# Kernel tuning notes

Measured on AMD Instinct MI355X. Metric: run time of the kernel, lower is better.

The kernel has to match this reference:

```python
import jax, jax.numpy as jnp
import numpy as np

NQ = 6   # n_qubits
NL = 6   # n_layers
B = 32768
TWO_PI = 6.2831853


def _ry(state, wire, theta):
    # state: [B, 2^NQ] complex64, wire 0 = most significant bit (torchquantum convention)
    b = state.shape[0]
    left, right = 2 ** wire, 2 ** (NQ - 1 - wire)
    s = state.reshape(b, left, 2, right)
    c = jnp.cos(theta * 0.5)[:, None, None].astype(state.dtype)
    sn = jnp.sin(theta * 0.5)[:, None, None].astype(state.dtype)
    s0, s1 = s[:, :, 0], s[:, :, 1]
    out = jnp.stack([c * s0 - sn * s1, sn * s0 + c * s1], axis=2)
    return out.reshape(b, -1)


def _rz(state, wire, theta):
    b = state.shape[0]
    left, right = 2 ** wire, 2 ** (NQ - 1 - wire)
    s = state.reshape(b, left, 2, right)
    p0 = jnp.exp(-0.5j * theta)[:, None, None].astype(state.dtype)
    p1 = jnp.exp(0.5j * theta)[:, None, None].astype(state.dtype)
    out = jnp.stack([s[:, :, 0] * p0, s[:, :, 1] * p1], axis=2)
    return out.reshape(b, -1)


def _cnot(state, ctrl, tgt):
    b = state.shape[0]
    s = state.reshape((b,) + (2,) * NQ)
    c_ax = ctrl + 1
    t_ax_in_slice = tgt + 1 if tgt < ctrl else tgt  # target axis after removing ctrl axis
    s0 = jnp.take(s, 0, axis=c_ax)
    s1 = jnp.flip(jnp.take(s, 1, axis=c_ax), axis=t_ax_in_slice)
    out = jnp.stack([s0, s1], axis=c_ax)
    return out.reshape(b, -1)


def _encode(x):
    # SphericalEncodingLayer: theta = acos(z), phi = atan2(y,x) mod 2pi; ry(theta), rz(phi) on each wire
    b = x.shape[0]
    theta = jnp.arccos(jnp.clip(x[:, 2], -1.0, 1.0))
    phi = jnp.mod(jnp.arctan2(x[:, 1], x[:, 0]) + TWO_PI, TWO_PI)
    state = jnp.zeros((b, 2 ** NQ), dtype=jnp.complex64).at[:, 0].set(1.0)
    for i in range(NQ):
        state = _ry(state, i, theta)
        state = _rz(state, i, phi)
    return state


def _qlayer(state, p):
    # BatchedQLayer: per wire rz(p[:,2i]), ry(p[:,2i+1]); then CNOT ring
    for i in range(NQ):
        state = _rz(state, i, p[:, 2 * i])
        state = _ry(state, i, p[:, 2 * i + 1])
    for i in range(NQ - 1):
        state = _cnot(state, i, i + 1)
    state = _cnot(state, NQ - 1, 0)
    return state


def _pauli_z_signs():
    k = np.arange(2 ** NQ)
    bits = (k[None, :] >> (NQ - 1 - np.arange(NQ))[:, None]) & 1  # [NQ, 2^NQ]
    return jnp.asarray(1 - 2 * bits, dtype=jnp.float32)


def setup_inputs() -> dict:
    key = jax.random.key(0)
    k1, k2 = jax.random.split(key)
    x = jax.random.normal(k1, (B, 3), dtype=jnp.float32)
    x = x / jnp.linalg.norm(x, axis=1, keepdims=True)  # points on unit sphere
    weights = jax.random.uniform(k2, (B, NL * 2 * NQ), dtype=jnp.float32,
                                 minval=0.0, maxval=TWO_PI)
    return {"x": x, "weights": weights}


def reference(x, weights):
    state = _encode(x)
    pos = 0
    for _ in range(NL):
        state = _qlayer(state, weights[:, pos:pos + 2 * NQ])
        pos += 2 * NQ
    probs = jnp.abs(state) ** 2                      # [B, 2^NQ]
    exp_vals = probs @ _pauli_z_signs().T            # [B, NQ] MeasureAll(PauliZ)
    return jax.nn.sigmoid(exp_vals)                  # no classical post-processing
```

## Files before the change

### kernel.cpp

```cpp
#include <hip/hip_runtime.h>

#define NQ 6
#define NL 6
#define TSTRIDE 148


typedef float v2f __attribute__((ext_vector_type(2)));

template<int CTRL>
__device__ __forceinline__ float dppf(float x) {
    return __builtin_bit_cast(float,
        __builtin_amdgcn_update_dpp(0, __builtin_bit_cast(int, x), CTRL, 0xF, 0xF, true));
}
__device__ __forceinline__ float sx1(float x) { return dppf<0xB1>(x); }
__device__ __forceinline__ float sx2(float x) { return dppf<0x4E>(x); }
__device__ __forceinline__ float sx4(float x) { return dppf<0x1B>(dppf<0x141>(x)); }

__device__ __forceinline__ v2f fma2(v2f a, v2f b, v2f c) {
    return __builtin_elementwise_fma(a, b, c);
}
__device__ __forceinline__ v2f swap2(v2f a) { return __builtin_shufflevector(a, a, 1, 0); }

__device__ __forceinline__ v2f shuf2_1(v2f a) { return v2f{sx1(a.x), sx1(a.y)}; }
__device__ __forceinline__ v2f shuf2_2(v2f a) { return v2f{sx2(a.x), sx2(a.y)}; }
__device__ __forceinline__ v2f shuf2_4(v2f a) { return v2f{sx4(a.x), sx4(a.y)}; }

template<int Q>
__device__ __forceinline__ void rz2(v2f (&re)[4], v2f (&im)[4], float c, float s, int lane) {
    const v2f C = {c, c};
    if constexpr (Q < 3) {
        const int lm = 4 >> Q;
        const float s2 = (lane & lm) ? s : -s;
        const v2f S = {s2, s2};
        #pragma unroll
        for (int p = 0; p < 4; ++p) {
            const v2f nr = fma2(re[p], C, -(im[p] * S));
            im[p] = fma2(re[p], S, im[p] * C);
            re[p] = nr;
        }
    } else if constexpr (Q == 5) {
        const v2f S = {-s, s};
        #pragma unroll
        for (int p = 0; p < 4; ++p) {
            const v2f nr = fma2(re[p], C, -(im[p] * S));
            im[p] = fma2(re[p], S, im[p] * C);
            re[p] = nr;
        }
    } else {
        const v2f Sn = {-s, -s}, Sp = {s, s};
        #pragma unroll
        for (int p = 0; p < 4; ++p) {
            const v2f S = (((Q == 3) ? (p & 2) : (p & 1)) != 0) ? Sp : Sn;
            const v2f nr = fma2(re[p], C, -(im[p] * S));
            im[p] = fma2(re[p], S, im[p] * C);
            re[p] = nr;
        }
    }
}

template<int Q>
__device__ __forceinline__ void ry2(v2f (&re)[4], v2f (&im)[4], float c, float s, int lane) {
    const v2f C = {c, c};
    if constexpr (Q < 3) {
        const int lm = 4 >> Q;
        const float sg = (lane & lm) ? s : -s;
        const v2f SG = {sg, sg};
        #pragma unroll
        for (int p = 0; p < 4; ++p) {
            v2f ore, oim;
            if constexpr (Q == 0)      { ore = shuf2_4(re[p]); oim = shuf2_4(im[p]); }
            else if constexpr (Q == 1) { ore = shuf2_2(re[p]); oim = shuf2_2(im[p]); }
            else                       { ore = shuf2_1(re[p]); oim = shuf2_1(im[p]); }
            re[p] = fma2(C, re[p], SG * ore);
            im[p] = fma2(C, im[p], SG * oim);
        }
    } else if constexpr (Q == 3) {
        const v2f S = {s, s};
        #pragma unroll
        for (int p = 0; p < 2; ++p) {
            const v2f a0r = re[p], a0i = im[p], a1r = re[p+2], a1i = im[p+2];
            re[p]   = fma2(C, a0r, -(S * a1r));
            im[p]   = fma2(C, a0i, -(S * a1i));
            re[p+2] = fma2(S, a0r, C * a1r);
            im[p+2] = fma2(S, a0i, C * a1i);
        }
    } else if constexpr (Q == 4) {
        const v2f S = {s, s};
        #pragma unroll
        for (int p = 0; p < 4; p += 2) {
            const v2f a0r = re[p], a0i = im[p], a1r = re[p+1], a1i = im[p+1];
            re[p]   = fma2(C, a0r, -(S * a1r));
            im[p]   = fma2(C, a0i, -(S * a1i));
            re[p+1] = fma2(S, a0r, C * a1r);
            im[p+1] = fma2(S, a0i, C * a1i);
        }
    } else {
        const v2f SM = {-s, s};
        #pragma unroll
        for (int p = 0; p < 4; ++p) {
            re[p] = fma2(C, re[p], SM * swap2(re[p]));
            im[p] = fma2(C, im[p], SM * swap2(im[p]));
        }
    }
}

__device__ __forceinline__ void cnot_block(v2f (&re)[4], v2f (&im)[4], int lane) {
    const bool c01 = (lane & 4) != 0;
    #pragma unroll
    for (int p = 0; p < 4; ++p) {
        const v2f dr = shuf2_2(re[p]), di = shuf2_2(im[p]);
        re[p] = c01 ? dr : re[p];
        im[p] = c01 ? di : im[p];
    }
    const bool c12 = (lane & 2) != 0;
    #pragma unroll
    for (int p = 0; p < 4; ++p) {
        const v2f dr = shuf2_1(re[p]), di = shuf2_1(im[p]);
        re[p] = c12 ? dr : re[p];
        im[p] = c12 ? di : im[p];
    }
    const bool c23 = (lane & 1) != 0;
    #pragma unroll
    for (int p = 0; p < 2; ++p) {
        const v2f ar = re[p], ai = im[p], br = re[p+2], bi = im[p+2];
        re[p]   = c23 ? br : ar;  im[p]   = c23 ? bi : ai;
        re[p+2] = c23 ? ar : br;  im[p+2] = c23 ? ai : bi;
    }
    { v2f t;
      t = re[2]; re[2] = re[3]; re[3] = t;
      t = im[2]; im[2] = im[3]; im[3] = t; }
    re[1] = swap2(re[1]); im[1] = swap2(im[1]);
    re[3] = swap2(re[3]); im[3] = swap2(im[3]);
    #pragma unroll
    for (int p = 0; p < 4; ++p) {
        re[p].y = sx4(re[p].y);
        im[p].y = sx4(im[p].y);
    }
}

__global__ __launch_bounds__(256) void qsim_kernel(
    const float* __restrict__ x,
    const float* __restrict__ w,
    float* __restrict__ out,
    int batch)
{
    __shared__ float tbl[32 * TSTRIDE];
    __shared__ float outbuf[4][48];

    const int tid   = threadIdx.x;
    const int wavei = tid >> 6;
    const int lane  = tid & 63;
    const int sw    = lane >> 3;
    const int g     = lane & 7;
    const int S     = tid >> 3;
    const int b     = blockIdx.x * 32 + S;
    if (b >= batch) return;

    float* T = &tbl[S * TSTRIDE];

    {
        const float* wp = w + (size_t)b * (2 * NQ * NL);
        #pragma unroll
        for (int j = 0; j < 9; ++j) {
            const int A = g * 9 + j;
            float s, c;
            __sincosf(wp[A] * 0.5f, &s, &c);
            const int word = (A >> 1) * 4 + (A & 1) * 2;
            T[word]     = c;
            T[word + 1] = s;
        }
    }

    const float x0 = x[b * 3 + 0];
    const float x1 = x[b * 3 + 1];
    const float x2 = x[b * 3 + 2];
    const float z  = fminf(1.f, fmaxf(-1.f, x2));
    const float ct = sqrtf(0.5f * (1.f + z));
    const float st = sqrtf(0.5f * (1.f - z));
    const float rr = sqrtf(x0 * x0 + x1 * x1) + 1e-30f;
    const float cphi = x0 / rr;
    const float cp = sqrtf(fmaxf(0.f, 0.5f * (1.f + cphi)));
    float sp       = sqrtf(fmaxf(0.f, 0.5f * (1.f - cphi)));
    sp = (x1 < 0.f) ? -sp : sp;

    const float Ar = ct * cp, Ai = -ct * sp;
    const float Br = st * cp, Bi =  st * sp;

    float pr[7], pi_[7], qr[7], qi[7];
    pr[0] = 1.f; pi_[0] = 0.f; qr[0] = 1.f; qi[0] = 0.f;
    pr[1] = Ar;  pi_[1] = Ai;  qr[1] = Br;  qi[1] = Bi;
    #pragma unroll
    for (int p = 2; p <= 6; ++p) {
        pr[p]  = fmaf(pr[p-1], Ar, -(pi_[p-1] * Ai));
        pi_[p] = fmaf(pr[p-1], Ai,  pi_[p-1] * Ar);
        qr[p]  = fmaf(qr[p-1], Br, -(qi[p-1] * Bi));
        qi[p]  = fmaf(qr[p-1], Bi,  qi[p-1] * Br);
    }
    float cr[7], ci[7];
    #pragma unroll
    for (int p = 0; p <= 6; ++p) {
        cr[p] = fmaf(pr[6-p], qr[p], -(pi_[6-p] * qi[p]));
        ci[p] = fmaf(pr[6-p], qi[p],  pi_[6-p] * qr[p]);
    }
    const int  pg = __popc(g);
    const bool pb0 = (pg & 1) != 0, pb1 = (pg & 2) != 0;
    float ur[4], ui[4];
    #pragma unroll
    for (int j = 0; j < 4; ++j) {
        const float lr  = pb0 ? cr[j+1] : cr[j];
        const float li  = pb0 ? ci[j+1] : ci[j];
        const float hr2 = pb0 ? cr[j+3] : cr[j+2];
        const float hi2 = pb0 ? ci[j+3] : ci[j+2];
        ur[j] = pb1 ? hr2 : lr;
        ui[j] = pb1 ? hi2 : li;
    }
    v2f re[4], im[4];
    re[0] = v2f{ur[0], ur[1]};  im[0] = v2f{ui[0], ui[1]};
    re[1] = v2f{ur[1], ur[2]};  im[1] = v2f{ui[1], ui[2]};
    re[2] = v2f{ur[1], ur[2]};  im[2] = v2f{ui[1], ui[2]};
    re[3] = v2f{ur[2], ur[3]};  im[3] = v2f{ui[2], ui[3]};

    for (int l = 0; l < NL - 1; ++l) {
        const float4 c0 = *(const float4*)&T[l*24 +  0];
        const float4 c1 = *(const float4*)&T[l*24 +  4];
        const float4 c2 = *(const float4*)&T[l*24 +  8];
        const float4 c3 = *(const float4*)&T[l*24 + 12];
        const float4 c4 = *(const float4*)&T[l*24 + 16];
        const float4 c5 = *(const float4*)&T[l*24 + 20];
        rz2<0>(re, im, c0.x, c0.y, lane);  ry2<0>(re, im, c0.z, c0.w, lane);
        rz2<1>(re, im, c1.x, c1.y, lane);  ry2<1>(re, im, c1.z, c1.w, lane);
        rz2<2>(re, im, c2.x, c2.y, lane);  ry2<2>(re, im, c2.z, c2.w, lane);
        rz2<3>(re, im, c3.x, c3.y, lane);  ry2<3>(re, im, c3.z, c3.w, lane);
        rz2<4>(re, im, c4.x, c4.y, lane);  ry2<4>(re, im, c4.z, c4.w, lane);
        rz2<5>(re, im, c5.x, c5.y, lane);  ry2<5>(re, im, c5.z, c5.w, lane);
        cnot_block(re, im, lane);
    }
    {
        const int l = NL - 1;
        const float4 c0 = *(const float4*)&T[l*24 +  0];
        const float4 c1 = *(const float4*)&T[l*24 +  4];
        const float4 c2 = *(const float4*)&T[l*24 +  8];
        const float4 c3 = *(const float4*)&T[l*24 + 12];
        const float4 c4 = *(const float4*)&T[l*24 + 16];
        const float4 c5 = *(const float4*)&T[l*24 + 20];
        rz2<0>(re, im, c0.x, c0.y, lane);  ry2<0>(re, im, c0.z, c0.w, lane);
        rz2<1>(re, im, c1.x, c1.y, lane);  ry2<1>(re, im, c1.z, c1.w, lane);
        rz2<2>(re, im, c2.x, c2.y, lane);  ry2<2>(re, im, c2.z, c2.w, lane);
        rz2<3>(re, im, c3.x, c3.y, lane);  ry2<3>(re, im, c3.z, c3.w, lane);
        rz2<4>(re, im, c4.x, c4.y, lane);  ry2<4>(re, im, c4.z, c4.w, lane);
        rz2<5>(re, im, c5.x, c5.y, lane);  ry2<5>(re, im, c5.z, c5.w, lane);
    }

    v2f v[4];
    #pragma unroll
    for (int p = 0; p < 4; ++p) v[p] = fma2(re[p], re[p], im[p] * im[p]);
    {
        v2f a, bb;
        a = v[0]; bb = v[2]; v[0] = a + bb; v[2] = a - bb;
        a = v[1]; bb = v[3]; v[1] = a + bb; v[3] = a - bb;
    }
    {
        v2f a, bb;
        a = v[0]; bb = v[1]; v[0] = a + bb; v[1] = a - bb;
        a = v[2]; bb = v[3]; v[2] = a + bb; v[3] = a - bb;
    }
    {
        const v2f PM = {1.f, -1.f};
        #pragma unroll
        for (int p = 0; p < 4; ++p) v[p] = fma2(PM, v[p], swap2(v[p]));
    }
    {
        const float sg = (lane & 1) ? -1.f : 1.f;
        const v2f SG = {sg, sg};
        #pragma unroll
        for (int p = 0; p < 4; ++p) v[p] = fma2(SG, v[p], shuf2_1(v[p]));
    }
    {
        const float sg = (lane & 2) ? -1.f : 1.f;
        const v2f SG = {sg, sg};
        #pragma unroll
        for (int p = 0; p < 4; ++p) v[p] = fma2(SG, v[p], shuf2_2(v[p]));
    }
    {
        const float sg = (lane & 4) ? -1.f : 1.f;
        const v2f SG = {sg, sg};
        #pragma unroll
        for (int p = 0; p < 4; ++p) v[p] = fma2(SG, v[p], shuf2_4(v[p]));
    }

    if (g == 3) outbuf[wavei][sw * 6 + 0] = v[3].y;
    if (g == 6) outbuf[wavei][sw * 6 + 1] = v[0].x;
    if (g == 7) {
        outbuf[wavei][sw * 6 + 2] = v[0].x;
        outbuf[wavei][sw * 6 + 3] = v[2].x;
        outbuf[wavei][sw * 6 + 4] = v[3].x;
        outbuf[wavei][sw * 6 + 5] = v[3].y;
    }
    if (lane < 48) {
        const float ev = outbuf[wavei][lane];
        const long long oidx = (long long)(blockIdx.x * 32 + wavei * 8) * 6 + lane;
        if (oidx < (long long)batch * 6)
            out[oidx] = 1.f / (1.f + __expf(-ev));
    }
}

extern "C" void kernel_launch(void* const* d_in, const int* in_sizes, int n_in,
                              void* d_out, int out_size, void* d_ws, size_t ws_size,
                              hipStream_t stream) {
    const float* x = (const float*)d_in[0];
    const float* w = (const float*)d_in[1];
    float* out = (float*)d_out;
    const int batch = in_sizes[0] / 3;

    const int threads = 256;
    const int blocks = (batch + 31) / 32;
    qsim_kernel<<<blocks, threads, 0, stream>>>(x, w, out, batch);
}
```

Before: 26.23 us.

## Spread each sample's statevector over 16 lanes instead of 8

Each batch sample now uses 16 lanes holding 4 amplitudes each, down from 8 lanes holding 8. Gates on the top four qubits become cross-lane DPP shuffles, including a new row-half mirror shuffle, and the CNOT ring and measurement butterflies are rewritten to match. The launch bound now requests higher occupancy and blocks cover 16 samples, so there are twice as many blocks. This aims to cut per-thread register pressure and the serial dependency chain and to expose more parallelism, at the cost of more DPP traffic and duplicated per-sample encoding and sincos work across lanes.

```diff
diff --git a/kernel.cpp b/kernel.cpp
--- a/kernel.cpp
+++ b/kernel.cpp
@@ -15,145 +15,134 @@
 __device__ __forceinline__ float sx1(float x) { return dppf<0xB1>(x); }
 __device__ __forceinline__ float sx2(float x) { return dppf<0x4E>(x); }
 __device__ __forceinline__ float sx4(float x) { return dppf<0x1B>(dppf<0x141>(x)); }
+__device__ __forceinline__ float sx8(float x) { return dppf<0x128>(x); }
 
 __device__ __forceinline__ v2f fma2(v2f a, v2f b, v2f c) {
     return __builtin_elementwise_fma(a, b, c);
 }
 __device__ __forceinline__ v2f swap2(v2f a) { return __builtin_shufflevector(a, a, 1, 0); }
 
-__device__ __forceinline__ v2f shuf2_1(v2f a) { return v2f{sx1(a.x), sx1(a.y)}; }
-__device__ __forceinline__ v2f shuf2_2(v2f a) { return v2f{sx2(a.x), sx2(a.y)}; }
-__device__ __forceinline__ v2f shuf2_4(v2f a) { return v2f{sx4(a.x), sx4(a.y)}; }
+template<int M>
+__device__ __forceinline__ v2f shuf2(v2f a) {
+    if constexpr (M == 1) return v2f{sx1(a.x), sx1(a.y)};
+    else if constexpr (M == 2) return v2f{sx2(a.x), sx2(a.y)};
+    else if constexpr (M == 4) return v2f{sx4(a.x), sx4(a.y)};
+    else return v2f{sx8(a.x), sx8(a.y)};
+}
 
 template<int Q>
-__device__ __forceinline__ void rz2(v2f (&re)[4], v2f (&im)[4], float c, float s, int lane) {
+__device__ __forceinline__ void rz2(v2f (&re)[2], v2f (&im)[2], float c, float s, int L) {
     const v2f C = {c, c};
-    if constexpr (Q < 3) {
-        const int lm = 4 >> Q;
-        const float s2 = (lane & lm) ? s : -s;
+    if constexpr (Q < 4) {
+        const int lm = 8 >> Q;
+        const float s2 = (L & lm) ? s : -s;
         const v2f S = {s2, s2};
         #pragma unroll
-        for (int p = 0; p < 4; ++p) {
+        for (int p = 0; p < 2; ++p) {
             const v2f nr = fma2(re[p], C, -(im[p] * S));
             im[p] = fma2(re[p], S, im[p] * C);
             re[p] = nr;
         }
-    } else if constexpr (Q == 5) {
+    } else if constexpr (Q == 4) {
+        const v2f Sn = {-s, -s}, Sp = {s, s};
+        { const v2f nr = fma2(re[0], C, -(im[0] * Sn));
+          im[0] = fma2(re[0], Sn, im[0] * C); re[0] = nr; }
+        { const v2f nr = fma2(re[1], C, -(im[1] * Sp));
+          im[1] = fma2(re[1], Sp, im[1] * C); re[1] = nr; }
+    } else {
         const v2f S = {-s, s};
         #pragma unroll
-        for (int p = 0; p < 4; ++p) {
+        for (int p = 0; p < 2; ++p) {
             const v2f nr = fma2(re[p], C, -(im[p] * S));
             im[p] = fma2(re[p], S, im[p] * C);
             re[p] = nr;
         }
-    } else {
-        const v2f Sn = {-s, -s}, Sp = {s, s};
-        #pragma unroll
-        for (int p = 0; p < 4; ++p) {
-            const v2f S = (((Q == 3) ? (p & 2) : (p & 1)) != 0) ? Sp : Sn;
-            const v2f nr = fma2(re[p], C, -(im[p] * S));
-            im[p] = fma2(re[p], S, im[p] * C);
-            re[p] = nr;
-        }
     }
 }
 
 template<int Q>
-__device__ __forceinline__ void ry2(v2f (&re)[4], v2f (&im)[4], float c, float s, int lane) {
+__device__ __forceinline__ void ry2(v2f (&re)[2], v2f (&im)[2], float c, float s, int L) {
     const v2f C = {c, c};
-    if constexpr (Q < 3) {
-        const int lm = 4 >> Q;
-        const float sg = (lane & lm) ? s : -s;
+    if constexpr (Q < 4) {
+        const int lm = 8 >> Q;
+        const float sg = (L & lm) ? s : -s;
         const v2f SG = {sg, sg};
         #pragma unroll
-        for (int p = 0; p < 4; ++p) {
-            v2f ore, oim;
-            if constexpr (Q == 0)      { ore = shuf2_4(re[p]); oim = shuf2_4(im[p]); }
-            else if constexpr (Q == 1) { ore = shuf2_2(re[p]); oim = shuf2_2(im[p]); }
-            else                       { ore = shuf2_1(re[p]); oim = shuf2_1(im[p]); }
+        for (int p = 0; p < 2; ++p) {
+            const v2f ore = shuf2<(8 >> Q)>(re[p]);
+            const v2f oim = shuf2<(8 >> Q)>(im[p]);
             re[p] = fma2(C, re[p], SG * ore);
             im[p] = fma2(C, im[p], SG * oim);
         }
-    } else if constexpr (Q == 3) {
-        const v2f S = {s, s};
-        #pragma unroll
-        for (int p = 0; p < 2; ++p) {
-            const v2f a0r = re[p], a0i = im[p], a1r = re[p+2], a1i = im[p+2];
-            re[p]   = fma2(C, a0r, -(S * a1r));
-            im[p]   = fma2(C, a0i, -(S * a1i));
-            re[p+2] = fma2(S, a0r, C * a1r);
-            im[p+2] = fma2(S, a0i, C * a1i);
-        }
     } else if constexpr (Q == 4) {
         const v2f S = {s, s};
-        #pragma unroll
-        for (int p = 0; p < 4; p += 2) {
-            const v2f a0r = re[p], a0i = im[p], a1r = re[p+1], a1i = im[p+1];
-            re[p]   = fma2(C, a0r, -(S * a1r));
-            im[p]   = fma2(C, a0i, -(S * a1i));
-            re[p+1] = fma2(S, a0r, C * a1r);
-            im[p+1] = fma2(S, a0i, C * a1i);
-        }
+        const v2f a0r = re[0], a0i = im[0], a1r = re[1], a1i = im[1];
+        re[0] = fma2(C, a0r, -(S * a1r));
+        im[0] = fma2(C, a0i, -(S * a1i));
+        re[1] = fma2(S, a0r, C * a1r);
+        im[1] = fma2(S, a0i, C * a1i);
     } else {
         const v2f SM = {-s, s};
         #pragma unroll
-        for (int p = 0; p < 4; ++p) {
+        for (int p = 0; p < 2; ++p) {
             re[p] = fma2(C, re[p], SM * swap2(re[p]));
             im[p] = fma2(C, im[p], SM * swap2(im[p]));
         }
     }
 }
 
-__device__ __forceinline__ void cnot_block(v2f (&re)[4], v2f (&im)[4], int lane) {
-    const bool c01 = (lane & 4) != 0;
-    #pragma unroll
-    for (int p = 0; p < 4; ++p) {
-        const v2f dr = shuf2_2(re[p]), di = shuf2_2(im[p]);
+__device__ __forceinline__ void cnot_block(v2f (&re)[2], v2f (&im)[2], int L) {
+    const bool c01 = (L & 8) != 0;
+    #pragma unroll
+    for (int p = 0; p < 2; ++p) {
+        const v2f dr = shuf2<4>(re[p]), di = shuf2<4>(im[p]);
         re[p] = c01 ? dr : re[p];
         im[p] = c01 ? di : im[p];
     }
-    const bool c12 = (lane & 2) != 0;
-    #pragma unroll
-    for (int p = 0; p < 4; ++p) {
-        const v2f dr = shuf2_1(re[p]), di = shuf2_1(im[p]);
+    const bool c12 = (L & 4) != 0;
+    #pragma unroll
+    for (int p = 0; p < 2; ++p) {
+        const v2f dr = shuf2<2>(re[p]), di = shuf2<2>(im[p]);
         re[p] = c12 ? dr : re[p];
         im[p] = c12 ? di : im[p];
     }
-    const bool c23 = (lane & 1) != 0;
-    #pragma unroll
-    for (int p = 0; p < 2; ++p) {
-        const v2f ar = re[p], ai = im[p], br = re[p+2], bi = im[p+2];
-        re[p]   = c23 ? br : ar;  im[p]   = c23 ? bi : ai;
-        re[p+2] = c23 ? ar : br;  im[p+2] = c23 ? ai : bi;
-    }
-    { v2f t;
-      t = re[2]; re[2] = re[3]; re[3] = t;
-      t = im[2]; im[2] = im[3]; im[3] = t; }
-    re[1] = swap2(re[1]); im[1] = swap2(im[1]);
-    re[3] = swap2(re[3]); im[3] = swap2(im[3]);
-    #pragma unroll
-    for (int p = 0; p < 4; ++p) {
-        re[p].y = sx4(re[p].y);
-        im[p].y = sx4(im[p].y);
-    }
-}
-
-__global__ __launch_bounds__(256) void qsim_kernel(
+    const bool c23 = (L & 2) != 0;
+    #pragma unroll
+    for (int p = 0; p < 2; ++p) {
+        const v2f dr = shuf2<1>(re[p]), di = shuf2<1>(im[p]);
+        re[p] = c23 ? dr : re[p];
+        im[p] = c23 ? di : im[p];
+    }
+    const bool c34 = (L & 1) != 0;
+    {
+        const v2f ar = re[0], ai = im[0], br = re[1], bi = im[1];
+        re[0] = c34 ? br : ar;  im[0] = c34 ? bi : ai;
+        re[1] = c34 ? ar : br;  im[1] = c34 ? ai : bi;
+    }
+    re[1] = swap2(re[1]);  im[1] = swap2(im[1]);
+    #pragma unroll
+    for (int p = 0; p < 2; ++p) {
+        re[p].y = sx8(re[p].y);
+        im[p].y = sx8(im[p].y);
+    }
+}
+
+__global__ __launch_bounds__(256, 8) void qsim_kernel(
     const float* __restrict__ x,
     const float* __restrict__ w,
     float* __restrict__ out,
     int batch)
 {
-    __shared__ float tbl[32 * TSTRIDE];
-    __shared__ float outbuf[4][48];
+    __shared__ float tbl[16 * TSTRIDE];
+    __shared__ float outbuf[4][24];
 
     const int tid   = threadIdx.x;
     const int wavei = tid >> 6;
     const int lane  = tid & 63;
-    const int sw    = lane >> 3;
-    const int g     = lane & 7;
-    const int S     = tid >> 3;
-    const int b     = blockIdx.x * 32 + S;
+    const int L     = lane & 15;
+    const int sw    = lane >> 4;
+    const int S     = tid >> 4;
+    const int b     = blockIdx.x * 16 + S;
     if (b >= batch) return;
 
     float* T = &tbl[S * TSTRIDE];
@@ -161,13 +150,15 @@
     {
         const float* wp = w + (size_t)b * (2 * NQ * NL);
         #pragma unroll
-        for (int j = 0; j < 9; ++j) {
-            const int A = g * 9 + j;
-            float s, c;
-            __sincosf(wp[A] * 0.5f, &s, &c);
-            const int word = (A >> 1) * 4 + (A & 1) * 2;
-            T[word]     = c;
-            T[word + 1] = s;
+        for (int j = 0; j < 5; ++j) {
+            const int A = L + 16 * j;
+            if (A < 72) {
+                float s, c;
+                __sincosf(wp[A] * 0.5f, &s, &c);
+                const int word = (A >> 1) * 4 + (A & 1) * 2;
+                T[word]     = c;
+                T[word + 1] = s;
+            }
         }
     }
 
@@ -202,106 +193,94 @@
         cr[p] = fmaf(pr[6-p], qr[p], -(pi_[6-p] * qi[p]));
         ci[p] = fmaf(pr[6-p], qi[p],  pi_[6-p] * qr[p]);
     }
-    const int  pg = __popc(g);
-    const bool pb0 = (pg & 1) != 0, pb1 = (pg & 2) != 0;
-    float ur[4], ui[4];
-    #pragma unroll
-    for (int j = 0; j < 4; ++j) {
-        const float lr  = pb0 ? cr[j+1] : cr[j];
-        const float li  = pb0 ? ci[j+1] : ci[j];
-        const float hr2 = pb0 ? cr[j+3] : cr[j+2];
-        const float hi2 = pb0 ? ci[j+3] : ci[j+2];
-        ur[j] = pb1 ? hr2 : lr;
-        ui[j] = pb1 ? hi2 : li;
-    }
-    v2f re[4], im[4];
+    const int  pg  = __popc(L);
+    const bool pb0 = (pg & 1) != 0, pb1 = (pg & 2) != 0, pb2 = (pg & 4) != 0;
+    float ur[3], ui[3];
+    #pragma unroll
+    for (int j = 0; j < 3; ++j) {
+        const float a01 = pb0 ? cr[j+1] : cr[j];
+        const float b01 = pb0 ? ci[j+1] : ci[j];
+        const float a23 = pb0 ? cr[j+3] : cr[j+2];
+        const float b23 = pb0 ? ci[j+3] : ci[j+2];
+        const float lor = pb1 ? a23 : a01;
+        const float loi = pb1 ? b23 : b01;
+        ur[j] = pb2 ? cr[j+4] : lor;
+        ui[j] = pb2 ? ci[j+4] : loi;
+    }
+    v2f re[2], im[2];
     re[0] = v2f{ur[0], ur[1]};  im[0] = v2f{ui[0], ui[1]};
     re[1] = v2f{ur[1], ur[2]};  im[1] = v2f{ui[1], ui[2]};
-    re[2] = v2f{ur[1], ur[2]};  im[2] = v2f{ui[1], ui[2]};
-    re[3] = v2f{ur[2], ur[3]};  im[3] = v2f{ui[2], ui[3]};
+
+    #define LAYER_GATES(l)                                                   \
+    do {                                                                     \
+        const float4 c0 = *(const float4*)&T[(l)*24 +  0];                   \
+        const float4 c1 = *(const float4*)&T[(l)*24 +  4];                   \
+        const float4 c2 = *(const float4*)&T[(l)*24 +  8];                   \
+        const float4 c3 = *(const float4*)&T[(l)*24 + 12];                   \
+        const float4 c4 = *(const float4*)&T[(l)*24 + 16];                   \
+        const float4 c5 = *(const float4*)&T[(l)*24 + 20];                   \
+        rz2<0>(re, im, c0.x, c0.y, L);  ry2<0>(re, im, c0.z, c0.w, L);       \
+        rz2<1>(re, im, c1.x, c1.y, L);  ry2<1>(re, im, c1.z, c1.w, L);       \
+        rz2<2>(re, im, c2.x, c2.y, L);  ry2<2>(re, im, c2.z, c2.w, L);       \
+        rz2<3>(re, im, c3.x, c3.y, L);  ry2<3>(re, im, c3.z, c3.w, L);       \
+        rz2<4>(re, im, c4.x, c4.y, L);  ry2<4>(re, im, c4.z, c4.w, L);       \
+        rz2<5>(re, im, c5.x, c5.y, L);  ry2<5>(re, im, c5.z, c5.w, L);       \
+    } while (0)
 
     for (int l = 0; l < NL - 1; ++l) {
-        const float4 c0 = *(const float4*)&T[l*24 +  0];
-        const float4 c1 = *(const float4*)&T[l*24 +  4];
-        const float4 c2 = *(const float4*)&T[l*24 +  8];
-        const float4 c3 = *(const float4*)&T[l*24 + 12];
-        const float4 c4 = *(const float4*)&T[l*24 + 16];
-        const float4 c5 = *(const float4*)&T[l*24 + 20];
-        rz2<0>(re, im, c0.x, c0.y, lane);  ry2<0>(re, im, c0.z, c0.w, lane);
-        rz2<1>(re, im, c1.x, c1.y, lane);  ry2<1>(re, im, c1.z, c1.w, lane);
-        rz2<2>(re, im, c2.x, c2.y, lane);  ry2<2>(re, im, c2.z, c2.w, lane);
-        rz2<3>(re, im, c3.x, c3.y, lane);  ry2<3>(re, im, c3.z, c3.w, lane);
-        rz2<4>(re, im, c4.x, c4.y, lane);  ry2<4>(re, im, c4.z, c4.w, lane);
-        rz2<5>(re, im, c5.x, c5.y, lane);  ry2<5>(re, im, c5.z, c5.w, lane);
-        cnot_block(re, im, lane);
-    }
-    {
-        const int l = NL - 1;
-        const float4 c0 = *(const float4*)&T[l*24 +  0];
-        const float4 c1 = *(const float4*)&T[l*24 +  4];
-        const float4 c2 = *(const float4*)&T[l*24 +  8];
-        const float4 c3 = *(const float4*)&T[l*24 + 12];
-        const float4 c4 = *(const float4*)&T[l*24 + 16];
-        const float4 c5 = *(const float4*)&T[l*24 + 20];
-        rz2<0>(re, im, c0.x, c0.y, lane);  ry2<0>(re, im, c0.z, c0.w, lane);
-        rz2<1>(re, im, c1.x, c1.y, lane);  ry2<1>(re, im, c1.z, c1.w, lane);
-        rz2<2>(re, im, c2.x, c2.y, lane);  ry2<2>(re, im, c2.z, c2.w, lane);
-        rz2<3>(re, im, c3.x, c3.y, lane);  ry2<3>(re, im, c3.z, c3.w, lane);
-        rz2<4>(re, im, c4.x, c4.y, lane);  ry2<4>(re, im, c4.z, c4.w, lane);
-        rz2<5>(re, im, c5.x, c5.y, lane);  ry2<5>(re, im, c5.z, c5.w, lane);
-    }
-
-    v2f v[4];
-    #pragma unroll
-    for (int p = 0; p < 4; ++p) v[p] = fma2(re[p], re[p], im[p] * im[p]);
-    {
-        v2f a, bb;
-        a = v[0]; bb = v[2]; v[0] = a + bb; v[2] = a - bb;
-        a = v[1]; bb = v[3]; v[1] = a + bb; v[3] = a - bb;
-    }
-    {
-        v2f a, bb;
-        a = v[0]; bb = v[1]; v[0] = a + bb; v[1] = a - bb;
-        a = v[2]; bb = v[3]; v[2] = a + bb; v[3] = a - bb;
+        LAYER_GATES(l);
+        cnot_block(re, im, L);
+    }
+    LAYER_GATES(NL - 1);
+
+    v2f v[2];
+    v[0] = fma2(re[0], re[0], im[0] * im[0]);
+    v[1] = fma2(re[1], re[1], im[1] * im[1]);
+    {
+        const v2f a = v[0], bb = v[1];
+        v[0] = a + bb; v[1] = a - bb;
     }
     {
         const v2f PM = {1.f, -1.f};
-        #pragma unroll
-        for (int p = 0; p < 4; ++p) v[p] = fma2(PM, v[p], swap2(v[p]));
-    }
-    {
-        const float sg = (lane & 1) ? -1.f : 1.f;
-        const v2f SG = {sg, sg};
-        #pragma unroll
-        for (int p = 0; p < 4; ++p) v[p] = fma2(SG, v[p], shuf2_1(v[p]));
-    }
-    {
-        const float sg = (lane & 2) ? -1.f : 1.f;
-        const v2f SG = {sg, sg};
-        #pragma unroll
-        for (int p = 0; p < 4; ++p) v[p] = fma2(SG, v[p], shuf2_2(v[p]));
-    }
-    {
-        const float sg = (lane & 4) ? -1.f : 1.f;
-        const v2f SG = {sg, sg};
-        #pragma unroll
-        for (int p = 0; p < 4; ++p) v[p] = fma2(SG, v[p], shuf2_4(v[p]));
-    }
-
-    if (g == 3) outbuf[wavei][sw * 6 + 0] = v[3].y;
-    if (g == 6) outbuf[wavei][sw * 6 + 1] = v[0].x;
-    if (g == 7) {
-        outbuf[wavei][sw * 6 + 2] = v[0].x;
-        outbuf[wavei][sw * 6 + 3] = v[2].x;
-        outbuf[wavei][sw * 6 + 4] = v[3].x;
-        outbuf[wavei][sw * 6 + 5] = v[3].y;
-    }
-    if (lane < 48) {
+        v[0] = fma2(PM, v[0], swap2(v[0]));
+        v[1] = fma2(PM, v[1], swap2(v[1]));
+    }
+    {
+        const float sg = (L & 1) ? -1.f : 1.f;  const v2f SG = {sg, sg};
+        v[0] = fma2(SG, v[0], shuf2<1>(v[0]));
+        v[1] = fma2(SG, v[1], shuf2<1>(v[1]));
+    }
+    {
+        const float sg = (L & 2) ? -1.f : 1.f;  const v2f SG = {sg, sg};
+        v[0] = fma2(SG, v[0], shuf2<2>(v[0]));
+        v[1] = fma2(SG, v[1], shuf2<2>(v[1]));
+    }
+    {
+        const float sg = (L & 4) ? -1.f : 1.f;  const v2f SG = {sg, sg};
+        v[0] = fma2(SG, v[0], shuf2<4>(v[0]));
+        v[1] = fma2(SG, v[1], shuf2<4>(v[1]));
+    }
+    {
+        const float sg = (L & 8) ? -1.f : 1.f;  const v2f SG = {sg, sg};
+        v[0] = fma2(SG, v[0], shuf2<8>(v[0]));
+        v[1] = fma2(SG, v[1], shuf2<8>(v[1]));
+    }
+
+    if (L == 7)  outbuf[wavei][sw * 6 + 0] = v[1].y;
+    if (L == 12) outbuf[wavei][sw * 6 + 1] = v[0].x;
+    if (L == 14) outbuf[wavei][sw * 6 + 2] = v[0].x;
+    if (L == 15) {
+        outbuf[wavei][sw * 6 + 3] = v[0].x;
+        outbuf[wavei][sw * 6 + 4] = v[1].x;
+        outbuf[wavei][sw * 6 + 5] = v[1].y;
+    }
+    if (lane < 24) {
         const float ev = outbuf[wavei][lane];
-        const long long oidx = (long long)(blockIdx.x * 32 + wavei * 8) * 6 + lane;
+        const long long oidx = (long long)(blockIdx.x * 16 + wavei * 4) * 6 + lane;
         if (oidx < (long long)batch * 6)
             out[oidx] = 1.f / (1.f + __expf(-ev));
     }
+    #undef LAYER_GATES
 }
 
 extern "C" void kernel_launch(void* const* d_in, const int* in_sizes, int n_in,
@@ -313,6 +292,6 @@
     const int batch = in_sizes[0] / 3;
 
     const int threads = 256;
-    const int blocks = (batch + 31) / 32;
+    const int blocks = (batch + 15) / 16;
     qsim_kernel<<<blocks, threads, 0, stream>>>(x, w, out, batch);
 }
```

New measurement: 40.83 us. 1.56x slower.
